# Optimization experiments

Measured on AMD Instinct MI355X. Metric: run time of the kernel, lower is better.

## Reference

```python
import jax, jax.numpy as jnp
import numpy as np

H = 2  # num_heads hardcoded in the torch module


def setup_inputs() -> dict:
    key = jax.random.key(0)
    ks = jax.random.split(key, 10)
    B, S, D = 8, 2048, 512
    s = 0.02
    return {
        "rgb": jax.random.normal(ks[0], (B, S, D), jnp.float32),
        "event": jax.random.normal(ks[1], (B, S, D), jnp.float32),
        "w_rgb": jax.random.normal(ks[2], (D, D), jnp.float32) * s,
        "b_rgb": jnp.zeros((D,), jnp.float32),
        "w_event": jax.random.normal(ks[3], (D, D), jnp.float32) * s,
        "b_event": jnp.zeros((D,), jnp.float32),
        "w_in": jax.random.normal(ks[4], (3 * D, D), jnp.float32) * s,   # packed QKV in_proj, torch layout
        "b_in": jnp.zeros((3 * D,), jnp.float32),
        "w_out": jax.random.normal(ks[5], (D, D), jnp.float32) * s,
        "b_out": jnp.zeros((D,), jnp.float32),
    }


def _mha(q_in, kv_in, w_in, b_in, w_out, b_out):
    """torch nn.MultiheadAttention with key==value==kv_in, batch-first math."""
    B, S, D = q_in.shape
    hd = D // H
    q = q_in @ w_in[:D].T + b_in[:D]
    k = kv_in @ w_in[D:2 * D].T + b_in[D:2 * D]
    v = kv_in @ w_in[2 * D:].T + b_in[2 * D:]
    q = q.reshape(B, S, H, hd) * (1.0 / np.sqrt(hd))
    k = k.reshape(B, S, H, hd)
    v = v.reshape(B, S, H, hd)
    scores = jnp.einsum('bqhd,bkhd->bhqk', q, k)          # [B,H,S,S]
    attn = jax.nn.softmax(scores, axis=-1)
    out = jnp.einsum('bhqk,bkhd->bqhd', attn, v).reshape(B, S, D)
    return out @ w_out.T + b_out


def reference(rgb, event, w_rgb, b_rgb, w_event, b_event, w_in, b_in, w_out, b_out):
    rgb_p = rgb @ w_rgb.T + b_rgb
    event_p = event @ w_event.T + b_event
    # same attention weights used for both cross directions
    event_attn = _mha(rgb_p, event_p, w_in, b_in, w_out, b_out)
    rgb_attn = _mha(event_p, rgb_p, w_in, b_in, w_out, b_out)
    gate = jax.nn.sigmoid(jnp.sum(rgb_p * event_p, axis=-1, keepdims=True))
    fused = gate * event_attn + (1.0 - gate) * rgb_attn
    return fused + (rgb_p + event_p) * 0.5
```

## Files before the change

kernel.cpp:

```cpp
#include <hip/hip_runtime.h>
#include <hip/hip_bf16.h>
#include <stdint.h>


typedef __bf16 bf16_t;
typedef __bf16 bf16x8 __attribute__((ext_vector_type(8)));
typedef float f32x4 __attribute__((ext_vector_type(4)));
typedef float f32x16 __attribute__((ext_vector_type(16)));
typedef unsigned int u32;

typedef void gvoid_t __attribute__((address_space(1)));
typedef void svoid_t __attribute__((address_space(3)));

__device__ inline void gload16(const void* g, void* l) {
    __builtin_amdgcn_global_load_lds((gvoid_t*)g, (svoid_t*)l, 16, 0, 0);
}

__device__ inline u32 cvtpk_bf16(float lo, float hi) {
    u32 r;
    asm("v_cvt_pk_bf16_f32 %0, %1, %2" : "=v"(r) : "v"(lo), "v"(hi));
    return r;
}

__global__ __launch_bounds__(256) void f2b_kernel(const float* __restrict__ in,
                                                  bf16_t* __restrict__ out, int n8) {
    int i = blockIdx.x * 256 + threadIdx.x;
    if (i >= n8) return;
    const float4* p = reinterpret_cast<const float4*>(in) + (size_t)i * 2;
    float4 a = p[0], b = p[1];
    bf16x8 o;
    o[0] = (bf16_t)a.x; o[1] = (bf16_t)a.y; o[2] = (bf16_t)a.z; o[3] = (bf16_t)a.w;
    o[4] = (bf16_t)b.x; o[5] = (bf16_t)b.y; o[6] = (bf16_t)b.z; o[7] = (bf16_t)b.w;
    reinterpret_cast<bf16x8*>(out)[i] = o;
}

template <int MODE>
__global__ __launch_bounds__(256) void gemm_bt(const bf16_t* __restrict__ A,
                                               const bf16_t* __restrict__ Bw,
                                               const float* __restrict__ bias,
                                               void* __restrict__ Cout,
                                               const bf16_t* __restrict__ r1,
                                               const bf16_t* __restrict__ r2,
                                               bf16_t* __restrict__ qdst,
                                               bf16_t* __restrict__ kdst,
                                               bf16_t* __restrict__ vdst,
                                               int M, int N, int K) {
    __shared__ __align__(16) bf16_t As[128][64];
    __shared__ __align__(16) bf16_t Bs[128][64];
    const int tid = threadIdx.x, lane = tid & 63, w = tid >> 6;
    const int l16 = lane & 15, l4 = lane >> 4;
    const int wm = w >> 1, wn = w & 1;
    const size_t a0 = (size_t)blockIdx.y * 128;
    const size_t b0 = (size_t)blockIdx.x * 128;
    f32x4 acc[4][4] = {};
    const int srow = w * 32 + (lane >> 3);
    const int scol = (lane & 7) * 8;
    for (int kt = 0; kt < K; kt += 64) {
        __syncthreads();
#pragma unroll
        for (int i = 0; i < 4; ++i) {
            gload16(A + (a0 + srow + i * 8) * (size_t)K + kt + scol, &As[w * 32 + i * 8][0]);
            gload16(Bw + (b0 + srow + i * 8) * (size_t)K + kt + scol, &Bs[w * 32 + i * 8][0]);
        }
        __syncthreads();
#pragma unroll
        for (int kk = 0; kk < 2; ++kk) {
            bf16x8 af[4], bfr[4];
#pragma unroll
            for (int mi = 0; mi < 4; ++mi)
                af[mi] = *reinterpret_cast<const bf16x8*>(&As[wm * 64 + mi * 16 + l16][kk * 32 + l4 * 8]);
#pragma unroll
            for (int ni = 0; ni < 4; ++ni)
                bfr[ni] = *reinterpret_cast<const bf16x8*>(&Bs[wn * 64 + ni * 16 + l16][kk * 32 + l4 * 8]);
#pragma unroll
            for (int mi = 0; mi < 4; ++mi)
#pragma unroll
                for (int ni = 0; ni < 4; ++ni)
                    acc[mi][ni] = __builtin_amdgcn_mfma_f32_16x16x32_bf16(af[mi], bfr[ni], acc[mi][ni], 0, 0, 0);
        }
    }
#pragma unroll
    for (int mi = 0; mi < 4; ++mi) {
#pragma unroll
        for (int ni = 0; ni < 4; ++ni) {
            int col = (int)b0 + wn * 64 + ni * 16 + l16;
            float bs = bias[col];
            int row0 = (int)a0 + wm * 64 + mi * 16 + l4 * 4;
            float vv[4];
#pragma unroll
            for (int r = 0; r < 4; ++r) vv[r] = acc[mi][ni][r] + bs;
            if (MODE == 0) {
#pragma unroll
                for (int r = 0; r < 4; ++r)
                    ((bf16_t*)Cout)[(size_t)(row0 + r) * N + col] = (bf16_t)vv[r];
            } else if (MODE == 2) {
#pragma unroll
                for (int r = 0; r < 4; ++r) {
                    size_t idx = (size_t)(row0 + r) * N + col;
                    ((float*)Cout)[idx] = vv[r] + 0.5f * ((float)r1[idx] + (float)r2[idx]);
                }
            } else {
                if (col < 512) {
#pragma unroll
                    for (int r = 0; r < 4; ++r)
                        qdst[(size_t)(row0 + r) * 512 + col] = (bf16_t)(vv[r] * 0.0625f);
                } else if (col < 1024) {
                    int cc = col - 512, h = cc >> 8, d = cc & 255;
#pragma unroll
                    for (int r = 0; r < 4; ++r) {
                        int row = row0 + r;
                        int bh = (row >> 11) * 2 + h, seq = row & 2047;
                        kdst[((size_t)(bh * 64 + (seq >> 5))) * 8192 + (d >> 3) * 256 +
                             (seq & 31) * 8 + (d & 7)] = (bf16_t)vv[r];
                    }
                } else {
                    int cc = col - 1024, h = cc >> 8, d = cc & 255;
                    int bh = (row0 >> 11) * 2 + h, seq = row0 & 2047;
                    size_t idx = ((size_t)(bh * 64 + (seq >> 5))) * 8192 +
                                 ((seq >> 3) & 3) * 2048 + d * 8 + (seq & 7);
                    union { bf16_t h4[4]; uint2 u8; } pk;
#pragma unroll
                    for (int r = 0; r < 4; ++r) pk.h4[r] = (bf16_t)vv[r];
                    *reinterpret_cast<uint2*>(&vdst[idx]) = pk.u8;
                }
            }
        }
    }
}

__global__ __launch_bounds__(256) void gate_kernel(const bf16_t* __restrict__ rp,
                                                   const bf16_t* __restrict__ ep,
                                                   float* __restrict__ gate) {
    int row = blockIdx.x * 4 + (threadIdx.x >> 6);
    int lane = threadIdx.x & 63;
    bf16x8 a = reinterpret_cast<const bf16x8*>(rp + (size_t)row * 512)[lane];
    bf16x8 b = reinterpret_cast<const bf16x8*>(ep + (size_t)row * 512)[lane];
    float s = 0.f;
#pragma unroll
    for (int j = 0; j < 8; ++j) s += (float)a[j] * (float)b[j];
#pragma unroll
    for (int off = 32; off; off >>= 1) s += __shfl_xor(s, off, 64);
    if (lane == 0) gate[row] = 1.f / (1.f + __expf(-s));
}

__global__ __launch_bounds__(256, 2) void attn_kernel(const bf16_t* __restrict__ qbr,
                                                      const bf16_t* __restrict__ qbe,
                                                      const bf16_t* __restrict__ kbr,
                                                      const bf16_t* __restrict__ kbe,
                                                      const bf16_t* __restrict__ vbr,
                                                      const bf16_t* __restrict__ vbe,
                                                      bf16_t* __restrict__ out0,
                                                      bf16_t* __restrict__ out1) {
    __shared__ __align__(16) bf16_t smem[32768];
    const int bid = blockIdx.x;
    const int qb = bid >> 5;
    const int combo = bid & 31;
    const int dir = combo >> 4;
    const int bh = combo & 15;
    const int b = bh >> 1, h = bh & 1;
    const bf16_t* Qb = dir ? qbe : qbr;
    const bf16_t* Kc = dir ? kbr : kbe;
    const bf16_t* Vc = dir ? vbr : vbe;
    bf16_t* osrc = dir ? out1 : out0;
    const int tid = threadIdx.x;
    const int w = tid >> 6, l = tid & 63;
    const int l31 = l & 31, hi = l >> 5;
    const int q0w = qb * 128 + w * 32;

    const bf16_t* qp = Qb + ((size_t)(b * 2048 + q0w + l31)) * 512 + h * 256 + hi * 8;
    bf16x8 qf[16];
#pragma unroll
    for (int dch = 0; dch < 16; ++dch)
        qf[dch] = *reinterpret_cast<const bf16x8*>(qp + dch * 16);

    f32x16 O[8] = {};
    float mrun = -1e30f, lrun = 0.f;

    const bf16_t* kq = Kc + (size_t)bh * 524288 + (w * 2048 + l * 8);
    const bf16_t* vq = Vc + (size_t)bh * 524288 + (w * 2048 + l * 8);

#define STAGE(t, nb)                                              \
    do {                                                          \
        const bf16_t* ks_ = kq + (size_t)(t) * 8192;              \
        const bf16_t* vs_ = vq + (size_t)(t) * 8192;              \
        bf16_t* lk_ = &smem[(nb) * 16384 + w * 2048];             \
        bf16_t* lv_ = &smem[(nb) * 16384 + 8192 + w * 2048];      \
        gload16(ks_, lk_);                                        \
        gload16(ks_ + 512, lk_ + 512);                            \
        gload16(ks_ + 1024, lk_ + 1024);                          \
        gload16(ks_ + 1536, lk_ + 1536);                          \
        gload16(vs_, lv_);                                        \
        gload16(vs_ + 512, lv_ + 512);                            \
        gload16(vs_ + 1024, lv_ + 1024);                          \
        gload16(vs_ + 1536, lv_ + 1536);                          \
    } while (0)

    STAGE(0, 0);

    for (int kt2 = 0; kt2 < 64; ++kt2) {
        asm volatile("s_waitcnt vmcnt(0)" ::: "memory");
        __builtin_amdgcn_s_barrier();
        asm volatile("" ::: "memory");
        if (kt2 < 63) STAGE(kt2 + 1, (kt2 + 1) & 1);
        asm volatile("" ::: "memory");

        const int cb = kt2 & 1;
        const bf16_t* kb = &smem[cb * 16384 + hi * 256 + l31 * 8];
        const bf16_t* vb = &smem[cb * 16384 + 8192 + hi * 2048 + l31 * 8];

        f32x16 st = {};
#pragma unroll
        for (int dch = 0; dch < 16; ++dch) {
            bf16x8 kf = *reinterpret_cast<const bf16x8*>(kb + dch * 512);
            st = __builtin_amdgcn_mfma_f32_32x32x16_bf16(kf, qf[dch], st, 0, 0, 0);
        }

        float mx = -1e30f;
#pragma unroll
        for (int r = 0; r < 16; ++r) mx = fmaxf(mx, st[r]);
        mx = fmaxf(mx, __shfl_xor(mx, 32, 64));
        if (__any(mx - mrun > 8.f)) {
            float mnew = fmaxf(mrun, mx);
            float sc = __expf(mrun - mnew);
            mrun = mnew;
            lrun *= sc;
#pragma unroll
            for (int r = 0; r < 16; ++r) {
                int qr = (r & 3) + 8 * (r >> 2) + 4 * hi;
                float scr = __shfl(sc, qr, 64);
#pragma unroll
                for (int g = 0; g < 8; ++g) O[g][r] *= scr;
            }
        }
        float lsum = 0.f;
        u32 W[8];
#pragma unroll
        for (int m = 0; m < 8; ++m) {
            float plo = __expf(st[2 * m] - mrun);
            float phi_ = __expf(st[2 * m + 1] - mrun);
            lsum += plo + phi_;
            W[m] = cvtpk_bf16(plo, phi_);
        }
        lsum += __shfl_xor(lsum, 32, 64);
        lrun += lsum;

#pragma unroll
        for (int s = 0; s < 2; ++s) {
            u32 t0 = hi ? W[4 * s] : W[4 * s + 2];
            u32 t1 = hi ? W[4 * s + 1] : W[4 * s + 3];
            u32 r0 = (u32)__shfl_xor((int)t0, 32, 64);
            u32 r1 = (u32)__shfl_xor((int)t1, 32, 64);
            union { u32 uw[4]; bf16x8 v; } a;
            a.uw[0] = hi ? r0 : W[4 * s];
            a.uw[1] = hi ? r1 : W[4 * s + 1];
            a.uw[2] = hi ? W[4 * s + 2] : r0;
            a.uw[3] = hi ? W[4 * s + 3] : r1;
#pragma unroll
            for (int g = 0; g < 8; ++g) {
                bf16x8 vf = *reinterpret_cast<const bf16x8*>(vb + s * 4096 + g * 256);
                O[g] = __builtin_amdgcn_mfma_f32_32x32x16_bf16(a.v, vf, O[g], 0, 0, 0);
            }
        }
    }
#undef STAGE

#pragma unroll
    for (int r = 0; r < 16; ++r) {
        int qr = (r & 3) + 8 * (r >> 2) + 4 * hi;
        float linv = 1.0f / __shfl(lrun, qr, 64);
        size_t rowoff = ((size_t)(b * 2048 + q0w + qr)) * 512 + h * 256 + l31;
#pragma unroll
        for (int g = 0; g < 8; ++g)
            osrc[rowoff + g * 32] = (bf16_t)(O[g][r] * linv);
    }
}

__global__ __launch_bounds__(256) void mix_kernel(const bf16_t* __restrict__ a1,
                                                  const bf16_t* __restrict__ a2,
                                                  const float* __restrict__ gate,
                                                  bf16_t* __restrict__ outm) {
    int i = blockIdx.x * 256 + threadIdx.x;
    int m = i >> 6;
    float g = gate[m];
    bf16x8 x = reinterpret_cast<const bf16x8*>(a1)[i];
    bf16x8 y = reinterpret_cast<const bf16x8*>(a2)[i];
    bf16x8 o;
#pragma unroll
    for (int j = 0; j < 8; ++j) o[j] = (bf16_t)(g * (float)x[j] + (1.f - g) * (float)y[j]);
    reinterpret_cast<bf16x8*>(outm)[i] = o;
}

extern "C" void kernel_launch(void* const* d_in, const int* in_sizes, int n_in,
                              void* d_out, int out_size, void* d_ws, size_t ws_size,
                              hipStream_t stream) {
    const float* rgb = (const float*)d_in[0];
    const float* event = (const float*)d_in[1];
    const float* w_rgb = (const float*)d_in[2];
    const float* b_rgb = (const float*)d_in[3];
    const float* w_event = (const float*)d_in[4];
    const float* b_event = (const float*)d_in[5];
    const float* w_in = (const float*)d_in[6];
    const float* b_in = (const float*)d_in[7];
    const float* w_out = (const float*)d_in[8];
    const float* b_out = (const float*)d_in[9];
    float* out = (float*)d_out;

    const int M = 16384;
    const size_t MB16 = (size_t)16 * 1024 * 1024;
    char* ws = (char*)d_ws;
    bf16_t* wrgb_bf = (bf16_t*)(ws + 0);
    bf16_t* wevt_bf = (bf16_t*)(ws + 524288);
    bf16_t* wout_bf = (bf16_t*)(ws + 1048576);
    bf16_t* win_bf = (bf16_t*)(ws + 1572864);
    float* gate = (float*)(ws + 3145728);
    bf16_t* bufA = (bf16_t*)(ws + 4194304);
    bf16_t* bufB = (bf16_t*)(ws + 4194304 + MB16);
    bf16_t* rgbp = (bf16_t*)(ws + 4194304 + 2 * MB16);
    bf16_t* evtp = (bf16_t*)(ws + 4194304 + 3 * MB16);
    bf16_t* qbr  = (bf16_t*)(ws + 4194304 + 4 * MB16);
    bf16_t* qbe  = (bf16_t*)(ws + 4194304 + 5 * MB16);
    bf16_t* kbr  = (bf16_t*)(ws + 4194304 + 6 * MB16);
    bf16_t* kbe  = (bf16_t*)(ws + 4194304 + 7 * MB16);
    bf16_t* vbr  = (bf16_t*)(ws + 4194304 + 8 * MB16);
    bf16_t* vbe  = (bf16_t*)(ws + 4194304 + 9 * MB16);
    bf16_t* mixed = (bf16_t*)(ws + 4194304 + 10 * MB16);

    dim3 blk(256);
    f2b_kernel<<<4096, blk, 0, stream>>>(rgb, bufA, M * 512 / 8);
    f2b_kernel<<<4096, blk, 0, stream>>>(event, bufB, M * 512 / 8);
    f2b_kernel<<<128, blk, 0, stream>>>(w_rgb, wrgb_bf, 512 * 512 / 8);
    f2b_kernel<<<128, blk, 0, stream>>>(w_event, wevt_bf, 512 * 512 / 8);
    f2b_kernel<<<384, blk, 0, stream>>>(w_in, win_bf, 1536 * 512 / 8);
    f2b_kernel<<<128, blk, 0, stream>>>(w_out, wout_bf, 512 * 512 / 8);
    gemm_bt<0><<<dim3(4, 128), blk, 0, stream>>>(bufA, wrgb_bf, b_rgb, rgbp, nullptr, nullptr,
                                                 nullptr, nullptr, nullptr, M, 512, 512);
    gemm_bt<0><<<dim3(4, 128), blk, 0, stream>>>(bufB, wevt_bf, b_event, evtp, nullptr, nullptr,
                                                 nullptr, nullptr, nullptr, M, 512, 512);
    gate_kernel<<<4096, blk, 0, stream>>>(rgbp, evtp, gate);
    gemm_bt<1><<<dim3(12, 128), blk, 0, stream>>>(rgbp, win_bf, b_in, nullptr, nullptr, nullptr,
                                                  qbr, kbr, vbr, M, 1536, 512);
    gemm_bt<1><<<dim3(12, 128), blk, 0, stream>>>(evtp, win_bf, b_in, nullptr, nullptr, nullptr,
                                                  qbe, kbe, vbe, M, 1536, 512);
    attn_kernel<<<512, blk, 0, stream>>>(qbr, qbe, kbr, kbe, vbr, vbe, bufA, bufB);
    mix_kernel<<<4096, blk, 0, stream>>>(bufA, bufB, gate, mixed);
    gemm_bt<2><<<dim3(4, 128), blk, 0, stream>>>(mixed, wout_bf, b_out, out, rgbp, evtp,
                                                 nullptr, nullptr, nullptr, M, 512, 512);
}
```

Before: 374.1 us.

## Software-pipeline attention: overlap QK of next tile with softmax/PV of current

Restructures the flash-attention inner loop so the QK^T MFMAs for tile t+1 are interleaved with the PV MFMAs for tile t, with K and V staged in separately double-buffered LDS regions. The softmax scale now folds log2(e) into the Q scaling so the kernel can use the raw v_exp_f32 (exp2) instruction, and s_setprio is raised around the MFMA block. The aim is to hide softmax VALU latency and LDS load latency behind matrix-core work, at the cost of more live registers (two score accumulators) and more complex barrier sequencing.

```diff
diff --git a/kernel.cpp b/kernel.cpp
--- a/kernel.cpp
+++ b/kernel.cpp
@@ -19,6 +19,12 @@
 __device__ inline u32 cvtpk_bf16(float lo, float hi) {
     u32 r;
     asm("v_cvt_pk_bf16_f32 %0, %1, %2" : "=v"(r) : "v"(lo), "v"(hi));
+    return r;
+}
+
+__device__ inline float exp2v(float x) {
+    float r;
+    asm("v_exp_f32 %0, %1" : "=v"(r) : "v"(x));
     return r;
 }
 
@@ -103,7 +109,7 @@
                 if (col < 512) {
 #pragma unroll
                     for (int r = 0; r < 4; ++r)
-                        qdst[(size_t)(row0 + r) * 512 + col] = (bf16_t)(vv[r] * 0.0625f);
+                        qdst[(size_t)(row0 + r) * 512 + col] = (bf16_t)(vv[r] * 0.090168440f);
                 } else if (col < 1024) {
                     int cc = col - 512, h = cc >> 8, d = cc & 255;
 #pragma unroll
@@ -174,95 +180,156 @@
         qf[dch] = *reinterpret_cast<const bf16x8*>(qp + dch * 16);
 
     f32x16 O[8] = {};
+    f32x16 stA, stB;
     float mrun = -1e30f, lrun = 0.f;
+    union PA { u32 uw[4]; bf16x8 v; } pa0, pa1;
 
     const bf16_t* kq = Kc + (size_t)bh * 524288 + (w * 2048 + l * 8);
     const bf16_t* vq = Vc + (size_t)bh * 524288 + (w * 2048 + l * 8);
 
-#define STAGE(t, nb)                                              \
-    do {                                                          \
-        const bf16_t* ks_ = kq + (size_t)(t) * 8192;              \
-        const bf16_t* vs_ = vq + (size_t)(t) * 8192;              \
-        bf16_t* lk_ = &smem[(nb) * 16384 + w * 2048];             \
-        bf16_t* lv_ = &smem[(nb) * 16384 + 8192 + w * 2048];      \
-        gload16(ks_, lk_);                                        \
-        gload16(ks_ + 512, lk_ + 512);                            \
-        gload16(ks_ + 1024, lk_ + 1024);                          \
-        gload16(ks_ + 1536, lk_ + 1536);                          \
-        gload16(vs_, lv_);                                        \
-        gload16(vs_ + 512, lv_ + 512);                            \
-        gload16(vs_ + 1024, lv_ + 1024);                          \
-        gload16(vs_ + 1536, lv_ + 1536);                          \
-    } while (0)
-
-    STAGE(0, 0);
-
-    for (int kt2 = 0; kt2 < 64; ++kt2) {
-        asm volatile("s_waitcnt vmcnt(0)" ::: "memory");
-        __builtin_amdgcn_s_barrier();
-        asm volatile("" ::: "memory");
-        if (kt2 < 63) STAGE(kt2 + 1, (kt2 + 1) & 1);
-        asm volatile("" ::: "memory");
-
-        const int cb = kt2 & 1;
-        const bf16_t* kb = &smem[cb * 16384 + hi * 256 + l31 * 8];
-        const bf16_t* vb = &smem[cb * 16384 + 8192 + hi * 2048 + l31 * 8];
-
-        f32x16 st = {};
-#pragma unroll
-        for (int dch = 0; dch < 16; ++dch) {
-            bf16x8 kf = *reinterpret_cast<const bf16x8*>(kb + dch * 512);
-            st = __builtin_amdgcn_mfma_f32_32x32x16_bf16(kf, qf[dch], st, 0, 0, 0);
-        }
-
-        float mx = -1e30f;
-#pragma unroll
-        for (int r = 0; r < 16; ++r) mx = fmaxf(mx, st[r]);
-        mx = fmaxf(mx, __shfl_xor(mx, 32, 64));
-        if (__any(mx - mrun > 8.f)) {
-            float mnew = fmaxf(mrun, mx);
-            float sc = __expf(mrun - mnew);
-            mrun = mnew;
-            lrun *= sc;
-#pragma unroll
-            for (int r = 0; r < 16; ++r) {
-                int qr = (r & 3) + 8 * (r >> 2) + 4 * hi;
-                float scr = __shfl(sc, qr, 64);
-#pragma unroll
-                for (int g = 0; g < 8; ++g) O[g][r] *= scr;
-            }
-        }
-        float lsum = 0.f;
-        u32 W[8];
-#pragma unroll
-        for (int m = 0; m < 8; ++m) {
-            float plo = __expf(st[2 * m] - mrun);
-            float phi_ = __expf(st[2 * m + 1] - mrun);
-            lsum += plo + phi_;
-            W[m] = cvtpk_bf16(plo, phi_);
-        }
-        lsum += __shfl_xor(lsum, 32, 64);
-        lrun += lsum;
-
-#pragma unroll
-        for (int s = 0; s < 2; ++s) {
-            u32 t0 = hi ? W[4 * s] : W[4 * s + 2];
-            u32 t1 = hi ? W[4 * s + 1] : W[4 * s + 3];
-            u32 r0 = (u32)__shfl_xor((int)t0, 32, 64);
-            u32 r1 = (u32)__shfl_xor((int)t1, 32, 64);
-            union { u32 uw[4]; bf16x8 v; } a;
-            a.uw[0] = hi ? r0 : W[4 * s];
-            a.uw[1] = hi ? r1 : W[4 * s + 1];
-            a.uw[2] = hi ? W[4 * s + 2] : r0;
-            a.uw[3] = hi ? W[4 * s + 3] : r1;
-#pragma unroll
-            for (int g = 0; g < 8; ++g) {
-                bf16x8 vf = *reinterpret_cast<const bf16x8*>(vb + s * 4096 + g * 256);
-                O[g] = __builtin_amdgcn_mfma_f32_32x32x16_bf16(a.v, vf, O[g], 0, 0, 0);
-            }
-        }
+#define SK_(T, P)                                                      \
+    do {                                                               \
+        const bf16_t* s_ = kq + (size_t)(T) * 8192;                    \
+        bf16_t* d_ = &smem[(P) * 8192 + w * 2048];                     \
+        gload16(s_, d_); gload16(s_ + 512, d_ + 512);                  \
+        gload16(s_ + 1024, d_ + 1024); gload16(s_ + 1536, d_ + 1536);  \
+    } while (0)
+#define SV_(T, P)                                                      \
+    do {                                                               \
+        const bf16_t* s_ = vq + (size_t)(T) * 8192;                    \
+        bf16_t* d_ = &smem[16384 + (P) * 8192 + w * 2048];             \
+        gload16(s_, d_); gload16(s_ + 512, d_ + 512);                  \
+        gload16(s_ + 1024, d_ + 1024); gload16(s_ + 1536, d_ + 1536);  \
+    } while (0)
+
+#define SOFTMAX(STP)                                                          \
+    do {                                                                      \
+        float mx_ = STP[0];                                                   \
+        _Pragma("unroll") for (int r_ = 1; r_ < 16; ++r_)                     \
+            mx_ = fmaxf(mx_, STP[r_]);                                        \
+        mx_ = fmaxf(mx_, __shfl_xor(mx_, 32, 64));                            \
+        if (__any(mx_ - mrun > 8.f)) {                                        \
+            float mnew_ = fmaxf(mrun, mx_);                                   \
+            float sc_ = exp2v(mrun - mnew_);                                  \
+            mrun = mnew_; lrun *= sc_;                                        \
+            _Pragma("unroll") for (int r_ = 0; r_ < 16; ++r_) {               \
+                int qr_ = (r_ & 3) + 8 * (r_ >> 2) + 4 * hi;                  \
+                float scr_ = __shfl(sc_, qr_, 64);                            \
+                _Pragma("unroll") for (int g_ = 0; g_ < 8; ++g_)              \
+                    O[g_][r_] *= scr_;                                        \
+            }                                                                 \
+        }                                                                     \
+        float ls_ = 0.f;                                                      \
+        u32 W_[8];                                                            \
+        _Pragma("unroll") for (int m_ = 0; m_ < 8; ++m_) {                    \
+            float plo_ = exp2v(STP[2 * m_] - mrun);                           \
+            float phi_ = exp2v(STP[2 * m_ + 1] - mrun);                       \
+            ls_ += plo_ + phi_;                                               \
+            W_[m_] = cvtpk_bf16(plo_, phi_);                                  \
+        }                                                                     \
+        ls_ += __shfl_xor(ls_, 32, 64);                                       \
+        lrun += ls_;                                                          \
+        {                                                                     \
+            u32 t0_ = hi ? W_[0] : W_[2], t1_ = hi ? W_[1] : W_[3];           \
+            u32 r0_ = (u32)__shfl_xor((int)t0_, 32, 64);                      \
+            u32 r1_ = (u32)__shfl_xor((int)t1_, 32, 64);                      \
+            pa0.uw[0] = hi ? r0_ : W_[0]; pa0.uw[1] = hi ? r1_ : W_[1];       \
+            pa0.uw[2] = hi ? W_[2] : r0_; pa0.uw[3] = hi ? W_[3] : r1_;       \
+        }                                                                     \
+        {                                                                     \
+            u32 t0_ = hi ? W_[4] : W_[6], t1_ = hi ? W_[5] : W_[7];           \
+            u32 r0_ = (u32)__shfl_xor((int)t0_, 32, 64);                      \
+            u32 r1_ = (u32)__shfl_xor((int)t1_, 32, 64);                      \
+            pa1.uw[0] = hi ? r0_ : W_[4]; pa1.uw[1] = hi ? r1_ : W_[5];       \
+            pa1.uw[2] = hi ? W_[6] : r0_; pa1.uw[3] = hi ? W_[7] : r1_;       \
+        }                                                                     \
+    } while (0)
+
+#define QK_ONLY(STN, KPR)                                                     \
+    do {                                                                      \
+        const bf16_t* kb_ = &smem[(KPR) * 8192 + hi * 256 + l31 * 8];         \
+        _Pragma("unroll") for (int r_ = 0; r_ < 16; ++r_) STN[r_] = 0.f;      \
+        _Pragma("unroll") for (int d_ = 0; d_ < 16; ++d_) {                   \
+            bf16x8 kf_ = *reinterpret_cast<const bf16x8*>(kb_ + d_ * 512);    \
+            STN = __builtin_amdgcn_mfma_f32_32x32x16_bf16(kf_, qf[d_], STN, 0, 0, 0); \
+        }                                                                     \
+    } while (0)
+
+#define QKPV(STN, KPR, VPR)                                                   \
+    do {                                                                      \
+        const bf16_t* kb_ = &smem[(KPR) * 8192 + hi * 256 + l31 * 8];         \
+        const bf16_t* vb_ = &smem[16384 + (VPR) * 8192 + hi * 2048 + l31 * 8];\
+        _Pragma("unroll") for (int r_ = 0; r_ < 16; ++r_) STN[r_] = 0.f;      \
+        __builtin_amdgcn_s_setprio(1);                                        \
+        _Pragma("unroll") for (int i_ = 0; i_ < 8; ++i_) {                    \
+            bf16x8 k0_ = *reinterpret_cast<const bf16x8*>(kb_ + (2 * i_) * 512); \
+            STN = __builtin_amdgcn_mfma_f32_32x32x16_bf16(k0_, qf[2 * i_], STN, 0, 0, 0); \
+            bf16x8 v0_ = *reinterpret_cast<const bf16x8*>(vb_ + i_ * 256);    \
+            O[i_] = __builtin_amdgcn_mfma_f32_32x32x16_bf16(pa0.v, v0_, O[i_], 0, 0, 0); \
+            bf16x8 k1_ = *reinterpret_cast<const bf16x8*>(kb_ + (2 * i_ + 1) * 512); \
+            STN = __builtin_amdgcn_mfma_f32_32x32x16_bf16(k1_, qf[2 * i_ + 1], STN, 0, 0, 0); \
+            if (i_ > 0) {                                                     \
+                bf16x8 v1_ = *reinterpret_cast<const bf16x8*>(vb_ + 4096 + (i_ - 1) * 256); \
+                O[i_ - 1] = __builtin_amdgcn_mfma_f32_32x32x16_bf16(pa1.v, v1_, O[i_ - 1], 0, 0, 0); \
+            }                                                                 \
+        }                                                                     \
+        {                                                                     \
+            bf16x8 v1_ = *reinterpret_cast<const bf16x8*>(vb_ + 4096 + 7 * 256); \
+            O[7] = __builtin_amdgcn_mfma_f32_32x32x16_bf16(pa1.v, v1_, O[7], 0, 0, 0); \
+        }                                                                     \
+        __builtin_amdgcn_s_setprio(0);                                        \
+    } while (0)
+
+#define PV_ONLY(VPR)                                                          \
+    do {                                                                      \
+        const bf16_t* vb_ = &smem[16384 + (VPR) * 8192 + hi * 2048 + l31 * 8];\
+        _Pragma("unroll") for (int g_ = 0; g_ < 8; ++g_) {                    \
+            bf16x8 v0_ = *reinterpret_cast<const bf16x8*>(vb_ + g_ * 256);    \
+            O[g_] = __builtin_amdgcn_mfma_f32_32x32x16_bf16(pa0.v, v0_, O[g_], 0, 0, 0); \
+        }                                                                     \
+        _Pragma("unroll") for (int g_ = 0; g_ < 8; ++g_) {                    \
+            bf16x8 v1_ = *reinterpret_cast<const bf16x8*>(vb_ + 4096 + g_ * 256); \
+            O[g_] = __builtin_amdgcn_mfma_f32_32x32x16_bf16(pa1.v, v1_, O[g_], 0, 0, 0); \
+        }                                                                     \
+    } while (0)
+
+#define SYNC()                                              \
+    asm volatile("s_waitcnt vmcnt(0)" ::: "memory");        \
+    __builtin_amdgcn_s_barrier();
+
+    SK_(0, 0);
+    SYNC();
+    SK_(1, 1);
+    SV_(0, 0);
+    QK_ONLY(stA, 0);
+    for (int tb = 0; tb < 31; ++tb) {
+        const int t1 = 2 * tb + 1, t2 = 2 * tb + 2;
+        SYNC();
+        SK_(t1 + 1, 0);
+        SV_(t1, 1);
+        SOFTMAX(stA);
+        QKPV(stB, 1, 0);
+        SYNC();
+        SK_(t2 + 1, 1);
+        SV_(t2, 0);
+        SOFTMAX(stB);
+        QKPV(stA, 0, 1);
     }
-#undef STAGE
+    SYNC();
+    SV_(63, 1);
+    SOFTMAX(stA);
+    QKPV(stB, 1, 0);
+    SYNC();
+    SOFTMAX(stB);
+    PV_ONLY(1);
+
+#undef SK_
+#undef SV_
+#undef SOFTMAX
+#undef QK_ONLY
+#undef QKPV
+#undef PV_ONLY
+#undef SYNC
 
 #pragma unroll
     for (int r = 0; r < 16; ++r) {
```

Measured after the change: 377.0 us. Within noise of the previous version (+0.8%).
